# Optimization experiments

Measured on AMD Instinct MI355X. Metric: run time of the kernel, lower is better.

Reference implementation:

```python
import jax, jax.numpy as jnp
from jax import lax
import numpy as np

SCALES = 3
DIR_PROFILE = [2, 3, 4]


def _gaussian_lowpass():
    ks, sigma = 5, 1.0
    ax = np.arange(-ks // 2 + 1.0, ks // 2 + 1.0)
    g = np.exp(-0.5 * np.square(ax) / sigma ** 2)
    k1 = g / g.sum()
    k2 = np.outer(k1, k1)
    k2 = k2 / k2.sum()
    return k2.astype(np.float32)  # [5, 5]


def _oriented_filter(angle, scale):
    size = 15
    sx, sy = 2.0 * scale, 0.5 * scale
    x = np.arange(-size // 2 + 1, size // 2 + 1)
    y = np.arange(-size // 2 + 1, size // 2 + 1)
    X, Y = np.meshgrid(x, y)
    Xr = X * np.cos(angle) - Y * np.sin(angle)
    Yr = X * np.sin(angle) + Y * np.cos(angle)
    k = np.exp(-0.5 * (Xr ** 2 / sx ** 2 + Yr ** 2 / sy ** 2)) * Xr / sx ** 2
    k = k - k.mean()
    n = np.linalg.norm(k)
    if n > 1e-6:
        k = k / n
    return k.astype(np.float32)  # [15, 15]


LP_FILTER = jnp.asarray(_gaussian_lowpass())[None, None]  # [1,1,5,5]
DIR_FILTERS = []  # per scale: [n_dirs, 1, 15, 15]
for _s, _lvl in enumerate(DIR_PROFILE):
    _nd = 2 ** _lvl
    _fs = np.stack([_oriented_filter(np.pi * d / _nd, _s + 1) for d in range(_nd)])
    DIR_FILTERS.append(jnp.asarray(_fs)[:, None])


def _depthwise(x, kernel):
    # x: [N, 1, H, W]; kernel: [O, 1, kh, kw]; reflect-pad 'same' cross-correlation
    kh, kw = kernel.shape[2], kernel.shape[3]
    xp = jnp.pad(x, ((0, 0), (0, 0), (kh // 2, kh // 2), (kw // 2, kw // 2)), mode='reflect')
    return lax.conv_general_dilated(xp, kernel, (1, 1), 'VALID',
                                    dimension_numbers=('NCHW', 'OIHW', 'NCHW'))


def setup_inputs() -> dict:
    key = jax.random.key(0)
    x = jax.random.normal(key, (8, 3, 384, 384), dtype=jnp.float32)
    return {"x": x}


def reference(x) -> jnp.ndarray:
    B, C, H, W = x.shape
    xc = x.reshape(B * C, 1, H, W)  # each RGB channel processed independently

    # Non-subsampled Laplacian pyramid: bandpasses + final lowpass
    bandpasses = []
    current = xc
    for _ in range(SCALES):
        lp = _depthwise(current, LP_FILTER)
        bandpasses.append(current - lp)
        current = lp

    # Directional filter bank per scale (all directions in one grouped conv)
    feats = []
    for s in range(SCALES):
        feats.append(_depthwise(bandpasses[s], DIR_FILTERS[s]))  # [B*C, 2^lvl, H, W]
    feats.append(current)  # final lowpass [B*C, 1, H, W]

    out = jnp.concatenate(feats, axis=1)  # [B*C, 29, H, W]
    return out.reshape(B, C * out.shape[1], H, W)  # [B, 87, H, W]
```

## Files before the change

kernel.cpp:

```cpp
#include <hip/hip_runtime.h>

#define HH 384
#define WW 384
#define HWSZ (HH * WW)
#define NIMG 24

typedef float v2f __attribute__((ext_vector_type(2)));

__device__ __forceinline__ int refl(int i, int n) {
    if (i < 0) i = -i;
    if (i >= n) i = 2 * n - 2 - i;
    return i;
}

constexpr float LPW[5] = {
    0.054488684549642945f, 0.24420134200323332f, 0.40261994689424746f,
    0.24420134200323332f, 0.054488684549642945f
};

constexpr double CPI = 3.141592653589793;

constexpr double cexp(double x) {
    int k = 0; double t = x;
    while (t > 0.25 || t < -0.25) { t *= 0.5; ++k; }
    double sum = 1.0, term = 1.0;
    for (int n = 1; n <= 14; ++n) { term *= t / n; sum += term; }
    for (int i = 0; i < k; ++i) sum *= sum;
    return sum;
}
constexpr double ccos(double x) {
    double sgn = 1.0;
    if (x > CPI * 0.5) { x = CPI - x; sgn = -1.0; }
    double x2 = x * x, sum = 1.0, term = 1.0;
    for (int n = 1; n <= 12; ++n) { term *= -x2 / ((2.0 * n - 1) * (2.0 * n)); sum += term; }
    return sgn * sum;
}
constexpr double csin(double x) {
    if (x > CPI * 0.5) x = CPI - x;
    double x2 = x * x, sum = x, term = x;
    for (int n = 1; n <= 12; ++n) { term *= -x2 / ((2.0 * n) * (2.0 * n + 1)); sum += term; }
    return sum;
}
constexpr double csqrt(double x) {
    if (x <= 0.0) return 0.0;
    double y = x > 1.0 ? x : 1.0;
    for (int i = 0; i < 80; ++i) y = 0.5 * (y + x / y);
    return y;
}

struct F225 { double v[225]; };

constexpr F225 make_filter(int s, int d, int nd) {
    double angle = CPI * (double)d / (double)nd;
    double scale = (double)(s + 1);
    double sx = 2.0 * scale, sy = 0.5 * scale;
    double ca = ccos(angle), sa = csin(angle);
    F225 f{};
    double sum = 0.0;
    for (int r = 0; r < 15; ++r)
        for (int c = 0; c < 15; ++c) {
            double X = (double)(c - 7), Y = (double)(r - 7);
            double Xr = X * ca - Y * sa;
            double Yr = X * sa + Y * ca;
            double k = cexp(-0.5 * (Xr * Xr / (sx * sx) + Yr * Yr / (sy * sy))) * Xr / (sx * sx);
            f.v[r * 15 + c] = k; sum += k;
        }
    double mean = sum / 225.0;
    double ss = 0.0;
    for (int i = 0; i < 225; ++i) { f.v[i] -= mean; ss += f.v[i] * f.v[i]; }
    double n = csqrt(ss);
    if (n > 1e-6) for (int i = 0; i < 225; ++i) f.v[i] /= n;
    return f;
}

template <int S, int D>
struct Filt { static constexpr F225 v = make_filter(S, D, S == 0 ? 4 : (S == 1 ? 8 : 16)); };

constexpr const F225& getF(int s, int d) {
    if (s == 0) {
        if (d == 0) return Filt<0, 0>::v;
        if (d == 1) return Filt<0, 1>::v;
        return Filt<0, 2>::v;
    } else if (s == 1) {
        if (d == 0) return Filt<1, 0>::v;
        if (d == 1) return Filt<1, 1>::v;
        if (d == 2) return Filt<1, 2>::v;
        if (d == 3) return Filt<1, 3>::v;
        return Filt<1, 4>::v;
    } else {
        if (d == 0) return Filt<2, 0>::v;
        if (d == 1) return Filt<2, 1>::v;
        if (d == 2) return Filt<2, 2>::v;
        if (d == 3) return Filt<2, 3>::v;
        if (d == 4) return Filt<2, 4>::v;
        if (d == 5) return Filt<2, 5>::v;
        if (d == 6) return Filt<2, 6>::v;
        if (d == 7) return Filt<2, 7>::v;
        return Filt<2, 8>::v;
    }
}

template <int NH> struct PTab { float a[63 * NH]; float b[63 * NH]; };

template <int NH>
constexpr PTab<NH> make_ptab(int s) {
    PTab<NH> t{};
    for (int j = 0; j < 63; ++j) {
        int u, v;
        if (j < 7)       { u = 0;     v = j + 1; }
        else if (j < 14) { u = j - 6; v = 0;     }
        else { int p = j - 14; u = p / 7 + 1; v = p % 7 + 1; }
        for (int k = 0; k < NH; ++k) {
            int dP = (k == 0) ? NH : k;
            int dQ = (k == 0) ? 0 : k;
            const F225& FP = getF(s, dP);
            const F225& FQ = getF(s, dQ);
            double A = 0.5 * (FP.v[(7 + u) * 15 + (7 + v)] + FP.v[(7 + u) * 15 + (7 - v)]);
            double B = 0.5 * (FQ.v[(7 + u) * 15 + (7 + v)] - FQ.v[(7 + u) * 15 + (7 - v)]);
            t.a[j * NH + k] = (float)A;
            t.b[j * NH + k] = (float)B;
        }
    }
    return t;
}
template <int S, int NH>
struct PTbl { static constexpr PTab<NH> t = make_ptab<NH>(S); };

__device__ __forceinline__ v2f ld2(const float* p) {
    v2f r; r.x = p[0]; r.y = p[1]; return r;
}

constexpr unsigned fb(float f) { return __builtin_bit_cast(unsigned, f); }

template <unsigned B>
__device__ __forceinline__ void fmac(float& a, float s) {
    asm("v_fmac_f32 %0, %2, %1" : "+v"(a) : "v"(s), "n"(B));
}

template <int SIDX, int NH, int J, int K = 0>
__device__ __forceinline__ void accA(float (&P0)[NH], float (&P1)[NH],
                                     float sx, float sy) {
    if constexpr (K < NH) {
        constexpr unsigned b = fb(PTbl<SIDX, NH>::t.a[J * NH + K]);
        fmac<b>(P0[K], sx);
        fmac<b>(P1[K], sy);
        accA<SIDX, NH, J, K + 1>(P0, P1, sx, sy);
    }
}
template <int SIDX, int NH, int J, int K = 0>
__device__ __forceinline__ void accB(float (&Q0)[NH], float (&Q1)[NH],
                                     float dx, float dy) {
    if constexpr (K < NH) {
        constexpr unsigned b = fb(PTbl<SIDX, NH>::t.b[J * NH + K]);
        fmac<b>(Q0[K], dx);
        fmac<b>(Q1[K], dy);
        accB<SIDX, NH, J, K + 1>(Q0, Q1, dx, dy);
    }
}

template <int SIDX, int NH, int V = 1>
__device__ __forceinline__ void runH0(const float* r0,
                                      float (&Q0)[NH], float (&Q1)[NH]) {
    if constexpr (V <= 7) {
        v2f dv = ld2(r0 + V) - ld2(r0 - V);
        accB<SIDX, NH, V - 1>(Q0, Q1, dv.x, dv.y);
        runH0<SIDX, NH, V + 1>(r0, Q0, Q1);
    }
}

template <int SIDX, int NH, int U, int V = 1>
__device__ __forceinline__ void runV(const float* rp, const float* rm,
                                     float (&P0)[NH], float (&Q0)[NH],
                                     float (&P1)[NH], float (&Q1)[NH]) {
    if constexpr (V <= 7) {
        v2f a = ld2(rp + V);
        v2f b = ld2(rp - V);
        v2f c = ld2(rm + V);
        v2f d = ld2(rm - V);
        v2f t1 = a - d, t2 = b - c;
        v2f S = t1 + t2, D = t1 - t2;
        constexpr int J = 14 + (U - 1) * 7 + (V - 1);
        accA<SIDX, NH, J>(P0, P1, S.x, S.y);
        accB<SIDX, NH, J>(Q0, Q1, D.x, D.y);
        runV<SIDX, NH, U, V + 1>(rp, rm, P0, Q0, P1, Q1);
    }
}

template <int SIDX, int NH, int U = 1>
__device__ __forceinline__ void runU(const float* sm, int yb, int xc,
                                     float (&P0)[NH], float (&Q0)[NH],
                                     float (&P1)[NH], float (&Q1)[NH]) {
    if constexpr (U <= 7) {
        const float* rp = sm + (yb + U) * 49 + xc;
        const float* rm = sm + (yb - U) * 49 + xc;
        {
            v2f dvc = ld2(rp) - ld2(rm);
            accA<SIDX, NH, 6 + U>(P0, P1, dvc.x, dvc.y);
        }
        runV<SIDX, NH, U>(rp, rm, P0, Q0, P1, Q1);
        asm volatile("" ::: "memory");
        runU<SIDX, NH, U + 1>(sm, yb, xc, P0, Q0, P1, Q1);
    }
}

template <int SIDX, int NH>
__device__ __forceinline__ void dir_band(
    const float* sm, float* __restrict__ out, long nbase,
    int by, int bx, int lane, int c0) {
    int xg = (lane & 15) * 2;
    int yr = lane >> 4;
    int xc = xg + 7;
#pragma unroll 1
    for (int rr = 0; rr < 2; ++rr) {
        int yb = yr + 16 * rr + 7;
        float P0[NH], Q0[NH], P1[NH], Q1[NH];
#pragma unroll
        for (int k = 0; k < NH; ++k) { P0[k] = 0.f; Q0[k] = 0.f; P1[k] = 0.f; Q1[k] = 0.f; }

        runH0<SIDX, NH>(sm + yb * 49 + xc, Q0, Q1);
        asm volatile("" ::: "memory");
        runU<SIDX, NH>(sm, yb, xc, P0, Q0, P1, Q1);

        long idx = nbase + (long)c0 * HWSZ + (long)(by + yr + 16 * rr) * WW + bx + xg;
        out[idx] = Q0[0];
        out[idx + 1] = Q1[0];
        out[idx + (long)NH * HWSZ] = P0[0];
        out[idx + (long)NH * HWSZ + 1] = P1[0];
#pragma unroll
        for (int k = 1; k < NH; ++k) {
            out[idx + (long)k * HWSZ] = P0[k] + Q0[k];
            out[idx + (long)k * HWSZ + 1] = P1[k] + Q1[k];
            out[idx + (long)(2 * NH - k) * HWSZ] = P0[k] - Q0[k];
            out[idx + (long)(2 * NH - k) * HWSZ + 1] = P1[k] - Q1[k];
        }
    }
}

__global__ __launch_bounds__(256, 4) void nsst_fused(
    const float* __restrict__ x, float* __restrict__ out) {
    __shared__ float Xb[58 * 60];
    __shared__ float Tb[58 * 56];
    __shared__ float Pb[54 * 56];

    int n = blockIdx.z;
    int bx = blockIdx.x * 32, by = blockIdx.y * 32;
    int tx = threadIdx.x, ty = threadIdx.y;
    int lane = ty * 32 + tx;
    const float* ip = x + (long)n * HWSZ;
    long nbase = (long)n * 29 * HWSZ;

    for (int r = ty; r < 58; r += 8) {
        int gy = refl(by + r - 13, HH);
        for (int c = tx; c < 58; c += 32)
            Xb[r * 60 + c] = ip[(long)gy * WW + refl(bx + c - 13, WW)];
    }
    __syncthreads();
    for (int r = ty; r < 58; r += 8)
        for (int c = tx; c < 54; c += 32) {
            float s = 0.f;
#pragma unroll
            for (int i = 0; i < 5; ++i) s = fmaf(LPW[i], Xb[r * 60 + c + i], s);
            Tb[r * 56 + c] = s;
        }
    __syncthreads();
    for (int r = ty; r < 54; r += 8)
        for (int c = tx; c < 54; c += 32) {
            float s = 0.f;
#pragma unroll
            for (int i = 0; i < 5; ++i) s = fmaf(LPW[i], Tb[(r + i) * 56 + c], s);
            Pb[r * 56 + c] = s;
        }
    __syncthreads();
    for (int r = ty; r < 46; r += 8)
        for (int c = tx; c < 46; c += 32)
            Tb[r * 49 + c] = Xb[(r + 6) * 60 + c + 6] - Pb[(r + 4) * 56 + c + 4];
    __syncthreads();
    dir_band<0, 2>(Tb, out, nbase, by, bx, lane, 0);
    __syncthreads();
    for (int r = ty; r < 54; r += 8)
        for (int c = tx; c < 50; c += 32) {
            float s = 0.f;
#pragma unroll
            for (int i = 0; i < 5; ++i) s = fmaf(LPW[i], Pb[r * 56 + c + i], s);
            Tb[r * 52 + c] = s;
        }
    __syncthreads();
    for (int r = ty; r < 50; r += 8)
        for (int c = tx; c < 50; c += 32) {
            float s = 0.f;
#pragma unroll
            for (int i = 0; i < 5; ++i) s = fmaf(LPW[i], Tb[(r + i) * 52 + c], s);
            Xb[r * 52 + c] = s;
        }
    __syncthreads();
    for (int r = ty; r < 46; r += 8)
        for (int c = tx; c < 46; c += 32)
            Tb[r * 49 + c] = Pb[(r + 4) * 56 + c + 4] - Xb[(r + 2) * 52 + c + 2];
    __syncthreads();
    dir_band<1, 4>(Tb, out, nbase, by, bx, lane, 4);
    __syncthreads();
    for (int r = ty; r < 50; r += 8)
        for (int c = tx; c < 46; c += 32) {
            float s = 0.f;
#pragma unroll
            for (int i = 0; i < 5; ++i) s = fmaf(LPW[i], Xb[r * 52 + c + i], s);
            Tb[r * 48 + c] = s;
        }
    __syncthreads();
    for (int r = ty; r < 46; r += 8)
        for (int c = tx; c < 46; c += 32) {
            float s = 0.f;
#pragma unroll
            for (int i = 0; i < 5; ++i) s = fmaf(LPW[i], Tb[(r + i) * 48 + c], s);
            Pb[r * 48 + c] = s;
        }
    __syncthreads();
#pragma unroll
    for (int rr = 0; rr < 4; ++rr)
        out[nbase + 28l * HWSZ + (long)(by + ty + 8 * rr) * WW + bx + tx] =
            Pb[(ty + 8 * rr + 7) * 48 + tx + 7];
    for (int r = ty; r < 46; r += 8)
        for (int c = tx; c < 46; c += 32)
            Tb[r * 49 + c] = Xb[(r + 2) * 52 + c + 2] - Pb[r * 48 + c];
    __syncthreads();
    dir_band<2, 8>(Tb, out, nbase, by, bx, lane, 12);
}

extern "C" void kernel_launch(void* const* d_in, const int* in_sizes, int n_in,
                              void* d_out, int out_size, void* d_ws, size_t ws_size,
                              hipStream_t stream) {
    const float* x = (const float*)d_in[0];
    float* out = (float*)d_out;
    (void)d_ws; (void)ws_size;

    nsst_fused<<<dim3(12, 12, NIMG), dim3(32, 8), 0, stream>>>(x, out);
}
```

Before: 558.5 us.

## Use packed FMA with register row windows for more pixels per thread

```diff
diff --git a/kernel.cpp b/kernel.cpp
--- a/kernel.cpp
+++ b/kernel.cpp
@@ -126,112 +126,141 @@
 template <int S, int NH>
 struct PTbl { static constexpr PTab<NH> t = make_ptab<NH>(S); };
 
-__device__ __forceinline__ v2f ld2(const float* p) {
-    v2f r; r.x = p[0]; r.y = p[1]; return r;
-}
-
 constexpr unsigned fb(float f) { return __builtin_bit_cast(unsigned, f); }
-
-template <unsigned B>
-__device__ __forceinline__ void fmac(float& a, float s) {
-    asm("v_fmac_f32 %0, %2, %1" : "+v"(a) : "v"(s), "n"(B));
-}
-
-template <int SIDX, int NH, int J, int K = 0>
-__device__ __forceinline__ void accA(float (&P0)[NH], float (&P1)[NH],
-                                     float sx, float sy) {
-    if constexpr (K < NH) {
-        constexpr unsigned b = fb(PTbl<SIDX, NH>::t.a[J * NH + K]);
-        fmac<b>(P0[K], sx);
-        fmac<b>(P1[K], sy);
-        accA<SIDX, NH, J, K + 1>(P0, P1, sx, sy);
-    }
-}
-template <int SIDX, int NH, int J, int K = 0>
-__device__ __forceinline__ void accB(float (&Q0)[NH], float (&Q1)[NH],
-                                     float dx, float dy) {
-    if constexpr (K < NH) {
-        constexpr unsigned b = fb(PTbl<SIDX, NH>::t.b[J * NH + K]);
-        fmac<b>(Q0[K], dx);
-        fmac<b>(Q1[K], dy);
-        accB<SIDX, NH, J, K + 1>(Q0, Q1, dx, dy);
-    }
-}
-
-template <int SIDX, int NH, int V = 1>
-__device__ __forceinline__ void runH0(const float* r0,
-                                      float (&Q0)[NH], float (&Q1)[NH]) {
-    if constexpr (V <= 7) {
-        v2f dv = ld2(r0 + V) - ld2(r0 - V);
-        accB<SIDX, NH, V - 1>(Q0, Q1, dv.x, dv.y);
-        runH0<SIDX, NH, V + 1>(r0, Q0, Q1);
-    }
-}
-
-template <int SIDX, int NH, int U, int V = 1>
-__device__ __forceinline__ void runV(const float* rp, const float* rm,
-                                     float (&P0)[NH], float (&Q0)[NH],
-                                     float (&P1)[NH], float (&Q1)[NH]) {
-    if constexpr (V <= 7) {
-        v2f a = ld2(rp + V);
-        v2f b = ld2(rp - V);
-        v2f c = ld2(rm + V);
-        v2f d = ld2(rm - V);
-        v2f t1 = a - d, t2 = b - c;
-        v2f S = t1 + t2, D = t1 - t2;
-        constexpr int J = 14 + (U - 1) * 7 + (V - 1);
-        accA<SIDX, NH, J>(P0, P1, S.x, S.y);
-        accB<SIDX, NH, J>(Q0, Q1, D.x, D.y);
-        runV<SIDX, NH, U, V + 1>(rp, rm, P0, Q0, P1, Q1);
-    }
-}
-
-template <int SIDX, int NH, int U = 1>
-__device__ __forceinline__ void runU(const float* sm, int yb, int xc,
-                                     float (&P0)[NH], float (&Q0)[NH],
-                                     float (&P1)[NH], float (&Q1)[NH]) {
-    if constexpr (U <= 7) {
-        const float* rp = sm + (yb + U) * 49 + xc;
-        const float* rm = sm + (yb - U) * 49 + xc;
+constexpr unsigned long long fb2(float lo, float hi) {
+    return ((unsigned long long)fb(hi) << 32) | (unsigned long long)fb(lo);
+}
+
+template <unsigned long long C>
+__device__ __forceinline__ void pkfma_lo(v2f& acc, v2f sd) {
+    asm("v_pk_fma_f32 %0, %1, %2, %0 op_sel:[0,0,0] op_sel_hi:[0,1,1]"
+        : "+v"(acc) : "v"(sd), "s"(C));
+}
+template <unsigned long long C>
+__device__ __forceinline__ void pkfma_hi(v2f& acc, v2f sd) {
+    asm("v_pk_fma_f32 %0, %1, %2, %0 op_sel:[1,0,0] op_sel_hi:[1,1,1]"
+        : "+v"(acc) : "v"(sd), "s"(C));
+}
+
+template <int SIDX, int NH, int J, int PX, int K2 = 0>
+struct AccSD {
+    static __device__ __forceinline__ void run(v2f (&P)[PX][NH / 2], v2f (&Q)[PX][NH / 2],
+                                               const v2f (&sd)[PX]) {
+        constexpr unsigned long long CA = fb2(PTbl<SIDX, NH>::t.a[J * NH + 2 * K2],
+                                              PTbl<SIDX, NH>::t.a[J * NH + 2 * K2 + 1]);
+        constexpr unsigned long long CB = fb2(PTbl<SIDX, NH>::t.b[J * NH + 2 * K2],
+                                              PTbl<SIDX, NH>::t.b[J * NH + 2 * K2 + 1]);
+#pragma unroll
+        for (int j = 0; j < PX; ++j) pkfma_lo<CA>(P[j][K2], sd[j]);
+#pragma unroll
+        for (int j = 0; j < PX; ++j) pkfma_hi<CB>(Q[j][K2], sd[j]);
+        if constexpr (K2 + 1 < NH / 2) AccSD<SIDX, NH, J, PX, K2 + 1>::run(P, Q, sd);
+    }
+};
+template <int SIDX, int NH, int J, int PX, bool USEA, int K2 = 0>
+struct AccOne {
+    static __device__ __forceinline__ void run(v2f (&T)[PX][NH / 2], const v2f (&sd)[PX]) {
+        constexpr unsigned long long C = USEA
+            ? fb2(PTbl<SIDX, NH>::t.a[J * NH + 2 * K2], PTbl<SIDX, NH>::t.a[J * NH + 2 * K2 + 1])
+            : fb2(PTbl<SIDX, NH>::t.b[J * NH + 2 * K2], PTbl<SIDX, NH>::t.b[J * NH + 2 * K2 + 1]);
+#pragma unroll
+        for (int j = 0; j < PX; ++j) pkfma_lo<C>(T[j][K2], sd[j]);
+        if constexpr (K2 + 1 < NH / 2) AccOne<SIDX, NH, J, PX, USEA, K2 + 1>::run(T, sd);
+    }
+};
+
+template <int SIDX, int NH, int PX, int W, int V = 1>
+struct H0Step {
+    static __device__ __forceinline__ void run(const float (&w0)[W], v2f (&Q)[PX][NH / 2]) {
+        v2f sd[PX];
+#pragma unroll
+        for (int j = 0; j < PX; ++j) sd[j].x = w0[7 + V + j] - w0[7 - V + j];
+        AccOne<SIDX, NH, V - 1, PX, false>::run(Q, sd);
+        if constexpr (V < 7) H0Step<SIDX, NH, PX, W, V + 1>::run(w0, Q);
+    }
+};
+
+template <int SIDX, int NH, int PX, int W, int U, int V = 1>
+struct VStep {
+    static __device__ __forceinline__ void run(const float (&wp)[W], const float (&wm)[W],
+                                               v2f (&P)[PX][NH / 2], v2f (&Q)[PX][NH / 2]) {
+        v2f sd[PX];
+#pragma unroll
+        for (int j = 0; j < PX; ++j) {
+            float t1 = wp[7 + V + j] - wm[7 - V + j];
+            float t2 = wp[7 - V + j] - wm[7 + V + j];
+            sd[j].x = t1 + t2;
+            sd[j].y = t1 - t2;
+        }
+        AccSD<SIDX, NH, 14 + (U - 1) * 7 + (V - 1), PX>::run(P, Q, sd);
+        if constexpr (V < 7) VStep<SIDX, NH, PX, W, U, V + 1>::run(wp, wm, P, Q);
+    }
+};
+
+template <int SIDX, int NH, int PX, int W, int U = 1>
+struct UStep {
+    static __device__ __forceinline__ void run(const float* sm, int yb, int xg,
+                                               v2f (&P)[PX][NH / 2], v2f (&Q)[PX][NH / 2]) {
+        float wp[W], wm[W];
+#pragma unroll
+        for (int i = 0; i < W; ++i) wp[i] = sm[(yb + U) * 49 + xg + i];
+#pragma unroll
+        for (int i = 0; i < W; ++i) wm[i] = sm[(yb - U) * 49 + xg + i];
         {
-            v2f dvc = ld2(rp) - ld2(rm);
-            accA<SIDX, NH, 6 + U>(P0, P1, dvc.x, dvc.y);
-        }
-        runV<SIDX, NH, U>(rp, rm, P0, Q0, P1, Q1);
+            v2f sd[PX];
+#pragma unroll
+            for (int j = 0; j < PX; ++j) sd[j].x = wp[7 + j] - wm[7 + j];
+            AccOne<SIDX, NH, 6 + U, PX, true>::run(P, sd);
+        }
+        VStep<SIDX, NH, PX, W, U>::run(wp, wm, P, Q);
         asm volatile("" ::: "memory");
-        runU<SIDX, NH, U + 1>(sm, yb, xc, P0, Q0, P1, Q1);
-    }
-}
-
-template <int SIDX, int NH>
+        if constexpr (U < 7) UStep<SIDX, NH, PX, W, U + 1>::run(sm, yb, xg, P, Q);
+    }
+};
+
+template <int SIDX, int NH, int PX>
 __device__ __forceinline__ void dir_band(
     const float* sm, float* __restrict__ out, long nbase,
     int by, int bx, int lane, int c0) {
-    int xg = (lane & 15) * 2;
-    int yr = lane >> 4;
-    int xc = xg + 7;
+    constexpr int W = 14 + PX;
+    constexpr int LPR = 32 / PX;
+    int xg = (lane % LPR) * PX;
+    int yr = lane / LPR;
 #pragma unroll 1
-    for (int rr = 0; rr < 2; ++rr) {
-        int yb = yr + 16 * rr + 7;
-        float P0[NH], Q0[NH], P1[NH], Q1[NH];
-#pragma unroll
-        for (int k = 0; k < NH; ++k) { P0[k] = 0.f; Q0[k] = 0.f; P1[k] = 0.f; Q1[k] = 0.f; }
-
-        runH0<SIDX, NH>(sm + yb * 49 + xc, Q0, Q1);
+    for (int rr = 0; rr < 4 / PX; ++rr) {
+        int y = yr + 8 * PX * rr;
+        int yb = y + 7;
+        v2f P[PX][NH / 2], Q[PX][NH / 2];
+#pragma unroll
+        for (int j = 0; j < PX; ++j)
+#pragma unroll
+            for (int k = 0; k < NH / 2; ++k) {
+                P[j][k] = (v2f){0.f, 0.f};
+                Q[j][k] = (v2f){0.f, 0.f};
+            }
+        {
+            float w0[W];
+#pragma unroll
+            for (int i = 0; i < W; ++i) w0[i] = sm[yb * 49 + xg + i];
+            H0Step<SIDX, NH, PX, W>::run(w0, Q);
+        }
         asm volatile("" ::: "memory");
-        runU<SIDX, NH>(sm, yb, xc, P0, Q0, P1, Q1);
-
-        long idx = nbase + (long)c0 * HWSZ + (long)(by + yr + 16 * rr) * WW + bx + xg;
-        out[idx] = Q0[0];
-        out[idx + 1] = Q1[0];
-        out[idx + (long)NH * HWSZ] = P0[0];
-        out[idx + (long)NH * HWSZ + 1] = P1[0];
+        UStep<SIDX, NH, PX, W>::run(sm, yb, xg, P, Q);
+
+        long idx0 = nbase + (long)c0 * HWSZ + (long)(by + y) * WW + bx + xg;
+#pragma unroll
+        for (int j = 0; j < PX; ++j) out[idx0 + j] = Q[j][0].x;
+#pragma unroll
+        for (int j = 0; j < PX; ++j) out[idx0 + (long)NH * HWSZ + j] = P[j][0].x;
 #pragma unroll
         for (int k = 1; k < NH; ++k) {
-            out[idx + (long)k * HWSZ] = P0[k] + Q0[k];
-            out[idx + (long)k * HWSZ + 1] = P1[k] + Q1[k];
-            out[idx + (long)(2 * NH - k) * HWSZ] = P0[k] - Q0[k];
-            out[idx + (long)(2 * NH - k) * HWSZ + 1] = P1[k] - Q1[k];
+#pragma unroll
+            for (int j = 0; j < PX; ++j) {
+                float p = (k & 1) ? P[j][k >> 1].y : P[j][k >> 1].x;
+                float q = (k & 1) ? Q[j][k >> 1].y : Q[j][k >> 1].x;
+                out[idx0 + (long)k * HWSZ + j] = p + q;
+                out[idx0 + (long)(2 * NH - k) * HWSZ + j] = p - q;
+            }
         }
     }
 }
@@ -275,7 +304,7 @@
         for (int c = tx; c < 46; c += 32)
             Tb[r * 49 + c] = Xb[(r + 6) * 60 + c + 6] - Pb[(r + 4) * 56 + c + 4];
     __syncthreads();
-    dir_band<0, 2>(Tb, out, nbase, by, bx, lane, 0);
+    dir_band<0, 2, 4>(Tb, out, nbase, by, bx, lane, 0);
     __syncthreads();
     for (int r = ty; r < 54; r += 8)
         for (int c = tx; c < 50; c += 32) {
@@ -297,7 +326,7 @@
         for (int c = tx; c < 46; c += 32)
             Tb[r * 49 + c] = Pb[(r + 4) * 56 + c + 4] - Xb[(r + 2) * 52 + c + 2];
     __syncthreads();
-    dir_band<1, 4>(Tb, out, nbase, by, bx, lane, 4);
+    dir_band<1, 4, 4>(Tb, out, nbase, by, bx, lane, 4);
     __syncthreads();
     for (int r = ty; r < 50; r += 8)
         for (int c = tx; c < 46; c += 32) {
@@ -323,7 +352,7 @@
         for (int c = tx; c < 46; c += 32)
             Tb[r * 49 + c] = Xb[(r + 2) * 52 + c + 2] - Pb[r * 48 + c];
     __syncthreads();
-    dir_band<2, 8>(Tb, out, nbase, by, bx, lane, 12);
+    dir_band<2, 8, 2>(Tb, out, nbase, by, bx, lane, 12);
 }
 
 extern "C" void kernel_launch(void* const* d_in, const int* in_sizes, int n_in,
```

New measurement: 626.1 us. 1.12x slower.
